# Kernel optimization log

Measured on AMD Instinct MI355X. Metric: run time of the kernel, lower is better.

## Reference

```python
import jax, jax.numpy as jnp
import numpy as np

BETA = 0.95
THR = 1.0
SLOPE = 25.0


@jax.custom_vjp
def spike(x):
    # heaviside(x) with fast_sigmoid surrogate gradient (slope=25)
    return (x > 0).astype(x.dtype)

def _spike_fwd(x):
    return (x > 0).astype(x.dtype), x

def _spike_bwd(x, g):
    return (g / (SLOPE * jnp.abs(x) + 1.0) ** 2,)

spike.defvjp(_spike_fwd, _spike_bwd)


def setup_inputs() -> dict:
    key = jax.random.key(0)
    ks = jax.random.split(key, 16)
    T, B, D_in, H, C = 25, 128, 2048, 4096, 1000
    P_ACTIVE = 0.1

    def sparse_layer(kw, kb, km, fan_in, fan_out):
        bound = (6.0 / fan_in) ** 0.5  # kaiming_uniform with a=sqrt(5) -> U(-sqrt(6/fan_in)*?, ...); approx scale
        w = jax.random.uniform(kw, (fan_out, fan_in), minval=-bound, maxval=bound, dtype=jnp.float32)
        mask = (jax.random.uniform(km, (fan_out, fan_in)) < P_ACTIVE).astype(jnp.float32)
        # rescale rows by sqrt(fan_in / fan_in_active) on active weights
        fan_act = jnp.clip(mask.sum(axis=1, keepdims=True), 1.0, None)
        scale = jnp.where((fan_act > 0) & (fan_act < fan_in), (fan_in / fan_act) ** 0.5, 1.0)
        w = jnp.where(mask > 0, w * scale, w)
        fan_eff = jnp.maximum(mask.sum(axis=1).mean(), 1.0)
        b_bound = 1.0 / fan_eff ** 0.5
        b = jax.random.uniform(kb, (fan_out,), minval=-b_bound, maxval=b_bound, dtype=jnp.float32)
        return w, b, mask

    w1, b1, m1 = sparse_layer(ks[0], ks[1], ks[2], D_in, H)
    w2, b2, m2 = sparse_layer(ks[3], ks[4], ks[5], H, H)
    w3, b3, m3 = sparse_layer(ks[6], ks[7], ks[8], H, H)
    bo_bound = 1.0 / H ** 0.5
    w_out = jax.random.uniform(ks[9], (C, H), minval=-bo_bound, maxval=bo_bound, dtype=jnp.float32)
    b_out = jax.random.uniform(ks[10], (C,), minval=-bo_bound, maxval=bo_bound, dtype=jnp.float32)
    x_seq = jax.random.normal(ks[11], (T, B, D_in), dtype=jnp.float32)
    return {"x_seq": x_seq, "w1": w1, "b1": b1, "m1": m1, "w2": w2, "b2": b2, "m2": m2,
            "w3": w3, "b3": b3, "m3": m3, "w_out": w_out, "b_out": b_out}


def _lif(cur, mem):
    # snntorch Leaky, reset_mechanism='subtract': reset spike from PREVIOUS mem, detached
    reset = jax.lax.stop_gradient((mem > THR).astype(mem.dtype))
    mem_new = BETA * mem + cur - reset * THR
    spk = spike(mem_new - THR)
    return spk, mem_new


def reference(x_seq, w1, b1, m1, w2, b2, m2, w3, b3, m3, w_out, b_out):
    T, B, _ = x_seq.shape
    ew1 = w1 * m1  # effective weights cached once (math identical to per-step recompute)
    ew2 = w2 * m2
    ew3 = w3 * m3

    mem1 = jnp.zeros((B, ew1.shape[0]), x_seq.dtype)
    mem2 = jnp.zeros((B, ew2.shape[0]), x_seq.dtype)
    mem3 = jnp.zeros((B, ew3.shape[0]), x_seq.dtype)
    mem_o = jnp.zeros((B, w_out.shape[0]), x_seq.dtype)
    spk_sum = jnp.zeros((B, w_out.shape[0]), x_seq.dtype)

    def step(carry, x_t):
        mem1, mem2, mem3, mem_o, spk_sum = carry
        spk1, mem1 = _lif(x_t @ ew1.T + b1, mem1)
        spk2, mem2 = _lif(spk1 @ ew2.T + b2, mem2)
        spk3, mem3 = _lif(spk2 @ ew3.T + b3, mem3)
        spk_o, mem_o = _lif(spk3 @ w_out.T + b_out, mem_o)
        return (mem1, mem2, mem3, mem_o, spk_sum + spk_o), None

    (mem1, mem2, mem3, mem_o, spk_sum), _ = jax.lax.scan(
        step, (mem1, mem2, mem3, mem_o, spk_sum), x_seq)
    return spk_sum
```

## Files before the change

kernel.cpp:

```cpp
#include <hip/hip_runtime.h>

#define T_STEPS 25
#define BATCH   128
#define D_IN    2048
#define H_DIM   4096
#define C_DIM   1000
#define N_ALL   3200
#define GEMM_Q  320
#define P_K2048 7
#define P_K4096 13
#define WOT_LD  1024

typedef __attribute__((address_space(1))) const void gas_t;
typedef __attribute__((address_space(3))) void las_t;

__device__ __forceinline__ int panel_len(int rem) {
    return (rem >= 2 * GEMM_Q) ? GEMM_Q
         : (rem > GEMM_Q ? ((rem / 2 + 15) & ~15) : rem);
}

__global__ __launch_bounds__(256)
void tmask_k(float* __restrict__ dst, const float* __restrict__ src,
             const float* __restrict__ msk, int M, int K, int MT)
{
    __shared__ float t[32][33];
    const int tx = threadIdx.x, ty = threadIdx.y;
    const int k0 = blockIdx.x * 32, m0 = blockIdx.y * 32;
    #pragma unroll
    for (int i = 0; i < 4; ++i) {
        const int m = m0 + ty + 8 * i;
        float v = 0.f;
        if (m < M) {
            const size_t gi = (size_t)m * K + k0 + tx;
            v = src[gi];
            if (msk) v *= msk[gi];
        }
        t[ty + 8 * i][tx] = v;
    }
    __syncthreads();
    const int mc = m0 + tx;
    if (mc < MT) {
        #pragma unroll
        for (int i = 0; i < 4; ++i)
            dst[(size_t)(k0 + ty + 8 * i) * MT + mc] = t[tx][ty + 8 * i];
    }
}

#define FMA8(AS, R)                                                   \
    acc[R][0].x = fmaf(AS, bv0.x, acc[R][0].x);                       \
    acc[R][0].y = fmaf(AS, bv0.y, acc[R][0].y);                       \
    acc[R][0].z = fmaf(AS, bv0.z, acc[R][0].z);                       \
    acc[R][0].w = fmaf(AS, bv0.w, acc[R][0].w);                       \
    acc[R][1].x = fmaf(AS, bv1.x, acc[R][1].x);                       \
    acc[R][1].y = fmaf(AS, bv1.y, acc[R][1].y);                       \
    acc[R][1].z = fmaf(AS, bv1.z, acc[R][1].z);                       \
    acc[R][1].w = fmaf(AS, bv1.w, acc[R][1].w);

template<int RM>
__global__ __launch_bounds__(64)
void gemm_w(const float* __restrict__ AT, const float* __restrict__ B,
            float* __restrict__ part, int MT, int K, int ldb, int n0)
{
#pragma clang fp reassociate(off)
    constexpr int TM  = RM * 4;
    constexpr int NST = (TM == 16) ? 1 : 2;
    __shared__ __align__(16) float As[2][16][TM];
    const int lane = threadIdx.x;
    const int cg   = lane & 15;
    const int mq   = lane >> 4;
    const int m0   = blockIdx.y * TM;
    const int p    = blockIdx.x;

    int pstart = 0, rem = K, pl = panel_len(K);
    for (int i = 0; i < p; ++i) { pstart += pl; rem -= pl; pl = panel_len(rem); }
    const int nt = pl >> 4;

    float4 acc[RM][2];
    #pragma unroll
    for (int r = 0; r < RM; ++r) {
        acc[r][0] = make_float4(0.f, 0.f, 0.f, 0.f);
        acc[r][1] = make_float4(0.f, 0.f, 0.f, 0.f);
    }

    const float* bp = B + (size_t)pstart * ldb + n0 + cg * 8;
    const int akr = (TM == 16) ? (lane >> 2) : (lane >> 3);
    const int amq = (TM == 16) ? ((lane & 3) * 4) : ((lane & 7) * 4);

    {
        const float* g = AT + (size_t)(pstart + akr) * MT + m0 + amq;
        __builtin_amdgcn_global_load_lds((gas_t*)g, (las_t*)&As[0][0][0], 16, 0, 0);
        if constexpr (NST == 2)
            __builtin_amdgcn_global_load_lds((gas_t*)(g + 8 * (size_t)MT),
                                             (las_t*)&As[0][8][0], 16, 0, 0);
    }

    for (int ti = 0; ti < nt; ++ti) {
        const int k0 = pstart + (ti << 4);
        const int bf = ti & 1;
        float4 bq[16];

        #pragma unroll
        for (int kk = 0; kk < 8; ++kk) {
            bq[2 * kk]     = *(const float4*)(bp + (size_t)kk * ldb);
            bq[2 * kk + 1] = *(const float4*)(bp + (size_t)kk * ldb + 4);
        }
        if (ti + 1 < nt) {
            const float* g = AT + (size_t)(k0 + 16 + akr) * MT + m0 + amq;
            __builtin_amdgcn_global_load_lds((gas_t*)g, (las_t*)&As[bf ^ 1][0][0], 16, 0, 0);
            if constexpr (NST == 2) {
                __builtin_amdgcn_global_load_lds((gas_t*)(g + 8 * (size_t)MT),
                                                 (las_t*)&As[bf ^ 1][8][0], 16, 0, 0);
                asm volatile("s_waitcnt vmcnt(2)" ::: "memory");
            } else {
                asm volatile("s_waitcnt vmcnt(1)" ::: "memory");
            }
        } else {
            asm volatile("s_waitcnt vmcnt(0)" ::: "memory");
        }
        __builtin_amdgcn_sched_barrier(0);
        #pragma unroll
        for (int kk = 0; kk < 8; ++kk) {
            const float4 bv0 = bq[2 * kk], bv1 = bq[2 * kk + 1];
            #pragma unroll
            for (int r4 = 0; r4 < RM; r4 += 4) {
                const float4 av = *(const float4*)&As[bf][kk][mq * RM + r4];
                FMA8(av.x, r4 + 0)
                FMA8(av.y, r4 + 1)
                FMA8(av.z, r4 + 2)
                FMA8(av.w, r4 + 3)
            }
        }

        #pragma unroll
        for (int kk = 0; kk < 8; ++kk) {
            bq[2 * kk]     = *(const float4*)(bp + (size_t)(kk + 8) * ldb);
            bq[2 * kk + 1] = *(const float4*)(bp + (size_t)(kk + 8) * ldb + 4);
        }
        bp += (size_t)16 * ldb;
        asm volatile("s_waitcnt vmcnt(0)" ::: "memory");
        __builtin_amdgcn_sched_barrier(0);
        #pragma unroll
        for (int kk = 8; kk < 16; ++kk) {
            const float4 bv0 = bq[2 * (kk - 8)], bv1 = bq[2 * (kk - 8) + 1];
            #pragma unroll
            for (int r4 = 0; r4 < RM; r4 += 4) {
                const float4 av = *(const float4*)&As[bf][kk][mq * RM + r4];
                FMA8(av.x, r4 + 0)
                FMA8(av.y, r4 + 1)
                FMA8(av.z, r4 + 2)
                FMA8(av.w, r4 + 3)
            }
        }
    }

    const int mrow0 = m0 + mq * RM;
    #pragma unroll
    for (int r = 0; r < RM; ++r) {
        *(float4*)&part[((size_t)p * MT + mrow0 + r) * BATCH + cg * 8]     = acc[r][0];
        *(float4*)&part[((size_t)p * MT + mrow0 + r) * BATCH + cg * 8 + 4] = acc[r][1];
    }
}

__device__ __forceinline__ float lif1e(float c, float& m)
{
    const float r = (m > 1.0f) ? 1.0f : 0.0f;
    const float mn = __fsub_rn(__fadd_rn(__fmul_rn(0.95f, m), c), r);
    m = mn;
    return (mn > 1.0f) ? 1.0f : 0.0f;
}

__global__ __launch_bounds__(256)
void reduce_lif4(const float* __restrict__ part, int P, int Mdim,
                 const float* __restrict__ bias, float* __restrict__ mem,
                 float* __restrict__ spk)
{
#pragma clang fp reassociate(off)
    const int idx4 = blockIdx.x * 256 + threadIdx.x;
    const int idx = idx4 * 4;
    const size_t stride = (size_t)Mdim * BATCH;
    float4 tot = *(const float4*)&part[idx];
    for (int z = 1; z < P; ++z) {
        const float4 pv = *(const float4*)&part[(size_t)z * stride + idx];
        tot.x = __fadd_rn(tot.x, pv.x); tot.y = __fadd_rn(tot.y, pv.y);
        tot.z = __fadd_rn(tot.z, pv.z); tot.w = __fadd_rn(tot.w, pv.w);
    }
    const float bb = bias[idx >> 7];
    float4 mm = *(float4*)&mem[idx];
    float4 sp;
    sp.x = lif1e(__fadd_rn(tot.x, bb), mm.x);
    sp.y = lif1e(__fadd_rn(tot.y, bb), mm.y);
    sp.z = lif1e(__fadd_rn(tot.z, bb), mm.z);
    sp.w = lif1e(__fadd_rn(tot.w, bb), mm.w);
    *(float4*)&mem[idx] = mm;
    *(float4*)&spk[idx] = sp;
}

__global__ __launch_bounds__(256)
void reduce_lif_out4(const float* __restrict__ part, int P, int Mpad,
                     const float* __restrict__ bias, float* __restrict__ mem,
                     float* __restrict__ out)
{
#pragma clang fp reassociate(off)
    const int idx4 = blockIdx.x * 256 + threadIdx.x;
    if (idx4 >= (C_DIM * BATCH) / 4) return;
    const int idx = idx4 * 4;
    const int cc = idx >> 7, b = idx & 127;
    const size_t stride = (size_t)Mpad * BATCH;
    float4 tot = *(const float4*)&part[idx];
    for (int z = 1; z < P; ++z) {
        const float4 pv = *(const float4*)&part[(size_t)z * stride + idx];
        tot.x = __fadd_rn(tot.x, pv.x); tot.y = __fadd_rn(tot.y, pv.y);
        tot.z = __fadd_rn(tot.z, pv.z); tot.w = __fadd_rn(tot.w, pv.w);
    }
    const float bb = bias[cc];
    float4 mm = *(float4*)&mem[idx];
    float s;
    s = lif1e(__fadd_rn(tot.x, bb), mm.x); if (s > 0.f) out[(size_t)(b+0) * C_DIM + cc] += 1.0f;
    s = lif1e(__fadd_rn(tot.y, bb), mm.y); if (s > 0.f) out[(size_t)(b+1) * C_DIM + cc] += 1.0f;
    s = lif1e(__fadd_rn(tot.z, bb), mm.z); if (s > 0.f) out[(size_t)(b+2) * C_DIM + cc] += 1.0f;
    s = lif1e(__fadd_rn(tot.w, bb), mm.w); if (s > 0.f) out[(size_t)(b+3) * C_DIM + cc] += 1.0f;
    *(float4*)&mem[idx] = mm;
}

extern "C" void kernel_launch(void* const* d_in, const int* in_sizes, int n_in,
                              void* d_out, int out_size, void* d_ws, size_t ws_size,
                              hipStream_t stream)
{
    const float* x  = (const float*)d_in[0];
    const float* w1 = (const float*)d_in[1];
    const float* b1 = (const float*)d_in[2];
    const float* m1 = (const float*)d_in[3];
    const float* w2 = (const float*)d_in[4];
    const float* b2 = (const float*)d_in[5];
    const float* m2 = (const float*)d_in[6];
    const float* w3 = (const float*)d_in[7];
    const float* b3 = (const float*)d_in[8];
    const float* m3 = (const float*)d_in[9];
    const float* wo = (const float*)d_in[10];
    const float* bo = (const float*)d_in[11];
    float* out = (float*)d_out;
    float* ws  = (float*)d_ws;
    (void)in_sizes; (void)n_in; (void)ws_size;

    const size_t HB = (size_t)H_DIM * BATCH;
    const size_t CB = (size_t)C_DIM * BATCH;

    size_t off = 0;
    const size_t MEM1 = off; off += HB;
    const size_t MEM2 = off; off += HB;
    const size_t MEM3 = off; off += HB;
    const size_t MEMO = off; off += CB;
    const size_t stateFloats = off;
    const size_t SPK1 = off; off += HB;
    const size_t SPK2 = off; off += HB;
    const size_t SPK3 = off; off += HB;
    const size_t PART = off; off += (size_t)P_K4096 * HB;
    const size_t EWT1 = off; off += (size_t)D_IN * H_DIM;
    const size_t EWT2 = off; off += (size_t)H_DIM * H_DIM;
    const size_t EWT3 = off; off += (size_t)H_DIM * H_DIM;
    const size_t WOT  = off; off += (size_t)H_DIM * WOT_LD;
    const size_t XT   = off; off += (size_t)D_IN * N_ALL;

    hipMemsetAsync(d_ws, 0, stateFloats * sizeof(float), stream);
    hipMemsetAsync(d_out, 0, (size_t)out_size * sizeof(float), stream);

    {
        dim3 tb(32, 8);
        tmask_k<<<dim3(D_IN / 32, H_DIM / 32), tb, 0, stream>>>(ws + EWT1, w1, m1, H_DIM, D_IN, H_DIM);
        tmask_k<<<dim3(H_DIM / 32, H_DIM / 32), tb, 0, stream>>>(ws + EWT2, w2, m2, H_DIM, H_DIM, H_DIM);
        tmask_k<<<dim3(H_DIM / 32, H_DIM / 32), tb, 0, stream>>>(ws + EWT3, w3, m3, H_DIM, H_DIM, H_DIM);
        tmask_k<<<dim3(H_DIM / 32, WOT_LD / 32), tb, 0, stream>>>(ws + WOT, wo, nullptr, C_DIM, H_DIM, WOT_LD);
        tmask_k<<<dim3(D_IN / 32, N_ALL / 32), tb, 0, stream>>>(ws + XT, x, nullptr, N_ALL, D_IN, N_ALL);
    }

    const dim3 g1(P_K2048, H_DIM / 16);
    const dim3 g23(P_K4096, H_DIM / 32);
    const dim3 go(P_K4096, WOT_LD / 16);
    const int gLif4  = (int)(HB / 4 / 256);
    const int gLifO4 = (int)((CB / 4 + 255) / 256);

    for (int t = 0; t < T_STEPS; ++t) {
        gemm_w<4><<<g1, 64, 0, stream>>>(ws + EWT1, ws + XT, ws + PART,
                                         H_DIM, D_IN, N_ALL, t * BATCH);
        reduce_lif4<<<gLif4, 256, 0, stream>>>(ws + PART, P_K2048, H_DIM, b1, ws + MEM1, ws + SPK1);

        gemm_w<8><<<g23, 64, 0, stream>>>(ws + EWT2, ws + SPK1, ws + PART,
                                          H_DIM, H_DIM, BATCH, 0);
        reduce_lif4<<<gLif4, 256, 0, stream>>>(ws + PART, P_K4096, H_DIM, b2, ws + MEM2, ws + SPK2);

        gemm_w<8><<<g23, 64, 0, stream>>>(ws + EWT3, ws + SPK2, ws + PART,
                                          H_DIM, H_DIM, BATCH, 0);
        reduce_lif4<<<gLif4, 256, 0, stream>>>(ws + PART, P_K4096, H_DIM, b3, ws + MEM3, ws + SPK3);

        gemm_w<4><<<go, 64, 0, stream>>>(ws + WOT, ws + SPK3, ws + PART,
                                         WOT_LD, H_DIM, BATCH, 0);
        reduce_lif_out4<<<gLifO4, 256, 0, stream>>>(ws + PART, P_K4096, WOT_LD, bo, ws + MEMO, out);
    }
}
```

Measured before the change: 5.594 ms.

## Double-buffer B register loads across half-tiles and drop the 32-row GEMM variant

The GEMM kernel is rewritten to keep two register banks of B-operand loads. The next half-tile's B rows are prefetched while the current half is being multiplied, and waits use counted vmcnt instead of full drains. The RM=8 template is removed, so layers 2 and 3 now use 16-row tiles with twice as many blocks. This aims to hide global-load latency and raise occupancy, at the cost of more register pressure and B reloads across more blocks.

```diff
diff --git a/kernel.cpp b/kernel.cpp
--- a/kernel.cpp
+++ b/kernel.cpp
@@ -56,106 +56,88 @@
     acc[R][1].z = fmaf(AS, bv1.z, acc[R][1].z);                       \
     acc[R][1].w = fmaf(AS, bv1.w, acc[R][1].w);
 
-template<int RM>
 __global__ __launch_bounds__(64)
 void gemm_w(const float* __restrict__ AT, const float* __restrict__ B,
             float* __restrict__ part, int MT, int K, int ldb, int n0)
 {
 #pragma clang fp reassociate(off)
-    constexpr int TM  = RM * 4;
-    constexpr int NST = (TM == 16) ? 1 : 2;
-    __shared__ __align__(16) float As[2][16][TM];
+    __shared__ __align__(16) float As[2][16][16];
     const int lane = threadIdx.x;
     const int cg   = lane & 15;
     const int mq   = lane >> 4;
-    const int m0   = blockIdx.y * TM;
+    const int m0   = blockIdx.y * 16;
     const int p    = blockIdx.x;
 
     int pstart = 0, rem = K, pl = panel_len(K);
     for (int i = 0; i < p; ++i) { pstart += pl; rem -= pl; pl = panel_len(rem); }
     const int nt = pl >> 4;
 
-    float4 acc[RM][2];
-    #pragma unroll
-    for (int r = 0; r < RM; ++r) {
+    float4 acc[4][2];
+    #pragma unroll
+    for (int r = 0; r < 4; ++r) {
         acc[r][0] = make_float4(0.f, 0.f, 0.f, 0.f);
         acc[r][1] = make_float4(0.f, 0.f, 0.f, 0.f);
     }
 
     const float* bp = B + (size_t)pstart * ldb + n0 + cg * 8;
-    const int akr = (TM == 16) ? (lane >> 2) : (lane >> 3);
-    const int amq = (TM == 16) ? ((lane & 3) * 4) : ((lane & 7) * 4);
-
-    {
-        const float* g = AT + (size_t)(pstart + akr) * MT + m0 + amq;
-        __builtin_amdgcn_global_load_lds((gas_t*)g, (las_t*)&As[0][0][0], 16, 0, 0);
-        if constexpr (NST == 2)
-            __builtin_amdgcn_global_load_lds((gas_t*)(g + 8 * (size_t)MT),
-                                             (las_t*)&As[0][8][0], 16, 0, 0);
+    const int akr = lane >> 2, amq = (lane & 3) * 4;
+    const float* ap = AT + (size_t)(pstart + akr) * MT + m0 + amq;
+
+    float4 bqA[16], bqB[16];
+
+    __builtin_amdgcn_global_load_lds((gas_t*)ap, (las_t*)&As[0][0][0], 16, 0, 0);
+    ap += (size_t)16 * MT;
+    #pragma unroll
+    for (int kk = 0; kk < 8; ++kk) {
+        bqA[2 * kk]     = *(const float4*)(bp + (size_t)kk * ldb);
+        bqA[2 * kk + 1] = *(const float4*)(bp + (size_t)kk * ldb + 4);
     }
 
     for (int ti = 0; ti < nt; ++ti) {
-        const int k0 = pstart + (ti << 4);
         const int bf = ti & 1;
-        float4 bq[16];
+        const bool more = (ti + 1 < nt);
 
         #pragma unroll
         for (int kk = 0; kk < 8; ++kk) {
-            bq[2 * kk]     = *(const float4*)(bp + (size_t)kk * ldb);
-            bq[2 * kk + 1] = *(const float4*)(bp + (size_t)kk * ldb + 4);
-        }
-        if (ti + 1 < nt) {
-            const float* g = AT + (size_t)(k0 + 16 + akr) * MT + m0 + amq;
-            __builtin_amdgcn_global_load_lds((gas_t*)g, (las_t*)&As[bf ^ 1][0][0], 16, 0, 0);
-            if constexpr (NST == 2) {
-                __builtin_amdgcn_global_load_lds((gas_t*)(g + 8 * (size_t)MT),
-                                                 (las_t*)&As[bf ^ 1][8][0], 16, 0, 0);
-                asm volatile("s_waitcnt vmcnt(2)" ::: "memory");
-            } else {
-                asm volatile("s_waitcnt vmcnt(1)" ::: "memory");
+            bqB[2 * kk]     = *(const float4*)(bp + (size_t)(kk + 8) * ldb);
+            bqB[2 * kk + 1] = *(const float4*)(bp + (size_t)(kk + 8) * ldb + 4);
+        }
+        if (more) {
+            __builtin_amdgcn_global_load_lds((gas_t*)ap, (las_t*)&As[bf ^ 1][0][0], 16, 0, 0);
+            ap += (size_t)16 * MT;
+            asm volatile("s_waitcnt vmcnt(17)" ::: "memory");
+        } else {
+            asm volatile("s_waitcnt vmcnt(16)" ::: "memory");
+        }
+        #pragma unroll
+        for (int kk = 0; kk < 8; ++kk) {
+            const float4 av = *(const float4*)&As[bf][kk][mq * 4];
+            const float4 bv0 = bqA[2 * kk], bv1 = bqA[2 * kk + 1];
+            FMA8(av.x, 0) FMA8(av.y, 1) FMA8(av.z, 2) FMA8(av.w, 3)
+        }
+
+        if (more) {
+            #pragma unroll
+            for (int kk = 0; kk < 8; ++kk) {
+                bqA[2 * kk]     = *(const float4*)(bp + (size_t)(kk + 16) * ldb);
+                bqA[2 * kk + 1] = *(const float4*)(bp + (size_t)(kk + 16) * ldb + 4);
             }
+            asm volatile("s_waitcnt vmcnt(17)" ::: "memory");
         } else {
             asm volatile("s_waitcnt vmcnt(0)" ::: "memory");
         }
-        __builtin_amdgcn_sched_barrier(0);
-        #pragma unroll
-        for (int kk = 0; kk < 8; ++kk) {
-            const float4 bv0 = bq[2 * kk], bv1 = bq[2 * kk + 1];
-            #pragma unroll
-            for (int r4 = 0; r4 < RM; r4 += 4) {
-                const float4 av = *(const float4*)&As[bf][kk][mq * RM + r4];
-                FMA8(av.x, r4 + 0)
-                FMA8(av.y, r4 + 1)
-                FMA8(av.z, r4 + 2)
-                FMA8(av.w, r4 + 3)
-            }
-        }
-
-        #pragma unroll
-        for (int kk = 0; kk < 8; ++kk) {
-            bq[2 * kk]     = *(const float4*)(bp + (size_t)(kk + 8) * ldb);
-            bq[2 * kk + 1] = *(const float4*)(bp + (size_t)(kk + 8) * ldb + 4);
-        }
         bp += (size_t)16 * ldb;
-        asm volatile("s_waitcnt vmcnt(0)" ::: "memory");
-        __builtin_amdgcn_sched_barrier(0);
         #pragma unroll
         for (int kk = 8; kk < 16; ++kk) {
-            const float4 bv0 = bq[2 * (kk - 8)], bv1 = bq[2 * (kk - 8) + 1];
-            #pragma unroll
-            for (int r4 = 0; r4 < RM; r4 += 4) {
-                const float4 av = *(const float4*)&As[bf][kk][mq * RM + r4];
-                FMA8(av.x, r4 + 0)
-                FMA8(av.y, r4 + 1)
-                FMA8(av.z, r4 + 2)
-                FMA8(av.w, r4 + 3)
-            }
-        }
-    }
-
-    const int mrow0 = m0 + mq * RM;
-    #pragma unroll
-    for (int r = 0; r < RM; ++r) {
+            const float4 av = *(const float4*)&As[bf][kk][mq * 4];
+            const float4 bv0 = bqB[2 * (kk - 8)], bv1 = bqB[2 * (kk - 8) + 1];
+            FMA8(av.x, 0) FMA8(av.y, 1) FMA8(av.z, 2) FMA8(av.w, 3)
+        }
+    }
+
+    const int mrow0 = m0 + mq * 4;
+    #pragma unroll
+    for (int r = 0; r < 4; ++r) {
         *(float4*)&part[((size_t)p * MT + mrow0 + r) * BATCH + cg * 8]     = acc[r][0];
         *(float4*)&part[((size_t)p * MT + mrow0 + r) * BATCH + cg * 8 + 4] = acc[r][1];
     }
@@ -274,26 +256,26 @@
     }
 
     const dim3 g1(P_K2048, H_DIM / 16);
-    const dim3 g23(P_K4096, H_DIM / 32);
+    const dim3 g23(P_K4096, H_DIM / 16);
     const dim3 go(P_K4096, WOT_LD / 16);
     const int gLif4  = (int)(HB / 4 / 256);
     const int gLifO4 = (int)((CB / 4 + 255) / 256);
 
     for (int t = 0; t < T_STEPS; ++t) {
-        gemm_w<4><<<g1, 64, 0, stream>>>(ws + EWT1, ws + XT, ws + PART,
-                                         H_DIM, D_IN, N_ALL, t * BATCH);
+        gemm_w<<<g1, 64, 0, stream>>>(ws + EWT1, ws + XT, ws + PART,
+                                      H_DIM, D_IN, N_ALL, t * BATCH);
         reduce_lif4<<<gLif4, 256, 0, stream>>>(ws + PART, P_K2048, H_DIM, b1, ws + MEM1, ws + SPK1);
 
-        gemm_w<8><<<g23, 64, 0, stream>>>(ws + EWT2, ws + SPK1, ws + PART,
-                                          H_DIM, H_DIM, BATCH, 0);
+        gemm_w<<<g23, 64, 0, stream>>>(ws + EWT2, ws + SPK1, ws + PART,
+                                       H_DIM, H_DIM, BATCH, 0);
         reduce_lif4<<<gLif4, 256, 0, stream>>>(ws + PART, P_K4096, H_DIM, b2, ws + MEM2, ws + SPK2);
 
-        gemm_w<8><<<g23, 64, 0, stream>>>(ws + EWT3, ws + SPK2, ws + PART,
-                                          H_DIM, H_DIM, BATCH, 0);
+        gemm_w<<<g23, 64, 0, stream>>>(ws + EWT3, ws + SPK2, ws + PART,
+                                       H_DIM, H_DIM, BATCH, 0);
         reduce_lif4<<<gLif4, 256, 0, stream>>>(ws + PART, P_K4096, H_DIM, b3, ws + MEM3, ws + SPK3);
 
-        gemm_w<4><<<go, 64, 0, stream>>>(ws + WOT, ws + SPK3, ws + PART,
-                                         WOT_LD, H_DIM, BATCH, 0);
+        gemm_w<<<go, 64, 0, stream>>>(ws + WOT, ws + SPK3, ws + PART,
+                                      WOT_LD, H_DIM, BATCH, 0);
         reduce_lif_out4<<<gLifO4, 256, 0, stream>>>(ws + PART, P_K4096, WOT_LD, bo, ws + MEMO, out);
     }
 }
```

Measured after the change: 8.240 ms. 47.3% more time.
